# Optimization experiments

Hardware: AMD Instinct MI355X
Metric: run time of the kernel (lower is better)

## Reference

```python
import jax, jax.numpy as jnp
import numpy as np

LEVEL = 4
INV_SQRT2 = np.float32(0.7071067811865476)  # db1 (Haar) filter coefficient


def haar_dwt(x):
    # pywt db1 single-level DWT for even-length signals (symmetric mode reduces
    # to this for the 2-tap Haar filter): cA[k]=(x[2k]+x[2k+1])/sqrt2,
    # cD[k]=(x[2k]-x[2k+1])/sqrt2
    xe = x[..., 0::2]
    xo = x[..., 1::2]
    cA = (xe + xo) * INV_SQRT2
    cD = (xe - xo) * INV_SQRT2
    return cA, cD


def haar_idwt(cA, cD):
    # inverse: x[2k]=(cA+cD)/sqrt2, x[2k+1]=(cA-cD)/sqrt2, interleaved
    even = (cA + cD) * INV_SQRT2
    odd = (cA - cD) * INV_SQRT2
    out = jnp.stack([even, odd], axis=-1)  # [..., n/2, 2]
    return out.reshape(*cA.shape[:-1], cA.shape[-1] * 2)


def setup_inputs() -> dict:
    key = jax.random.key(0)
    x = jax.random.normal(key, (32, 512, 4096), dtype=jnp.float32)
    return {"x": x}


def reference(x):
    # pywt.wavedec(x, 'db1', level=4): recursive DWT on approximation coeffs
    cA = x
    details = []
    for _ in range(LEVEL):
        cA, cD = haar_dwt(cA)
        details.append(cD)
    # pywt.waverec: reconstruct from [cA_L, cD_L, ..., cD_1]
    for cD in reversed(details):
        cA = haar_idwt(cA, cD)
    return cA
```

## Files before the change

### kernel.cpp

```cpp
#include <hip/hip_runtime.h>


#define WBLK 16

__global__ __launch_bounds__(256) void wavelet_rt_kernel(
    const float4* __restrict__ in, float4* __restrict__ out, int nthreads) {
  int t = blockIdx.x * blockDim.x + threadIdx.x;
  if (t >= nthreads) return;

  const float S = 0.7071067811865476f;

  float v[16];
  #pragma unroll
  for (int k = 0; k < 4; ++k) {
    float4 r = in[t * 4 + k];
    v[4 * k + 0] = r.x; v[4 * k + 1] = r.y;
    v[4 * k + 2] = r.z; v[4 * k + 3] = r.w;
  }

  float a1[8], d1[8];
  #pragma unroll
  for (int i = 0; i < 8; ++i) {
    float e = v[2 * i], o = v[2 * i + 1];
    a1[i] = (e + o) * S;
    d1[i] = (e - o) * S;
  }
  float a2[4], d2[4];
  #pragma unroll
  for (int i = 0; i < 4; ++i) {
    float e = a1[2 * i], o = a1[2 * i + 1];
    a2[i] = (e + o) * S;
    d2[i] = (e - o) * S;
  }
  float a3[2], d3[2];
  #pragma unroll
  for (int i = 0; i < 2; ++i) {
    float e = a2[2 * i], o = a2[2 * i + 1];
    a3[i] = (e + o) * S;
    d3[i] = (e - o) * S;
  }
  float a4 = (a3[0] + a3[1]) * S;
  float d4 = (a3[0] - a3[1]) * S;

  float b3[2];
  b3[0] = (a4 + d4) * S;
  b3[1] = (a4 - d4) * S;
  float b2[4];
  #pragma unroll
  for (int i = 0; i < 2; ++i) {
    b2[2 * i + 0] = (b3[i] + d3[i]) * S;
    b2[2 * i + 1] = (b3[i] - d3[i]) * S;
  }
  float b1[8];
  #pragma unroll
  for (int i = 0; i < 4; ++i) {
    b1[2 * i + 0] = (b2[i] + d2[i]) * S;
    b1[2 * i + 1] = (b2[i] - d2[i]) * S;
  }
  float w[16];
  #pragma unroll
  for (int i = 0; i < 8; ++i) {
    w[2 * i + 0] = (b1[i] + d1[i]) * S;
    w[2 * i + 1] = (b1[i] - d1[i]) * S;
  }

  #pragma unroll
  for (int k = 0; k < 4; ++k) {
    float4 o4;
    o4.x = w[4 * k + 0]; o4.y = w[4 * k + 1];
    o4.z = w[4 * k + 2]; o4.w = w[4 * k + 3];
    out[t * 4 + k] = o4;
  }
}

extern "C" void kernel_launch(void* const* d_in, const int* in_sizes, int n_in,
                              void* d_out, int out_size, void* d_ws, size_t ws_size,
                              hipStream_t stream) {
  const float* x = (const float*)d_in[0];
  float* out = (float*)d_out;
  int nthreads = out_size / WBLK;
  int block = 256;
  int grid = (nthreads + block - 1) / block;
  wavelet_rt_kernel<<<grid, block, 0, stream>>>(
      (const float4*)x, (float4*)out, nthreads);
}
```

Baseline: 437.9 us.

## Split each 16-element Haar block across four lanes using wavefront shuffles

Each thread now handles one float4 instead of four, and the coarser DWT levels are computed across neighbouring lanes via __shfl_xor exchanges. This makes every global load and store fully coalesced across the wavefront instead of 64-byte strided per lane. It quadruples the thread count and adds shuffle and select instructions.

```diff
diff --git a/kernel.cpp b/kernel.cpp
--- a/kernel.cpp
+++ b/kernel.cpp
@@ -1,7 +1,5 @@
 #include <hip/hip_runtime.h>
 
-
-#define WBLK 16
 
 __global__ __launch_bounds__(256) void wavelet_rt_kernel(
     const float4* __restrict__ in, float4* __restrict__ out, int nthreads) {
@@ -9,68 +7,34 @@
   if (t >= nthreads) return;
 
   const float S = 0.7071067811865476f;
+  const int lane = threadIdx.x & 63;
 
-  float v[16];
-  #pragma unroll
-  for (int k = 0; k < 4; ++k) {
-    float4 r = in[t * 4 + k];
-    v[4 * k + 0] = r.x; v[4 * k + 1] = r.y;
-    v[4 * k + 2] = r.z; v[4 * k + 3] = r.w;
-  }
+  float4 r = in[t];
+  float v0 = r.x, v1 = r.y, v2 = r.z, v3 = r.w;
 
-  float a1[8], d1[8];
-  #pragma unroll
-  for (int i = 0; i < 8; ++i) {
-    float e = v[2 * i], o = v[2 * i + 1];
-    a1[i] = (e + o) * S;
-    d1[i] = (e - o) * S;
-  }
-  float a2[4], d2[4];
-  #pragma unroll
-  for (int i = 0; i < 4; ++i) {
-    float e = a1[2 * i], o = a1[2 * i + 1];
-    a2[i] = (e + o) * S;
-    d2[i] = (e - o) * S;
-  }
-  float a3[2], d3[2];
-  #pragma unroll
-  for (int i = 0; i < 2; ++i) {
-    float e = a2[2 * i], o = a2[2 * i + 1];
-    a3[i] = (e + o) * S;
-    d3[i] = (e - o) * S;
-  }
-  float a4 = (a3[0] + a3[1]) * S;
-  float d4 = (a3[0] - a3[1]) * S;
+  float a1_0 = (v0 + v1) * S, d1_0 = (v0 - v1) * S;
+  float a1_1 = (v2 + v3) * S, d1_1 = (v2 - v3) * S;
+  float a2 = (a1_0 + a1_1) * S, d2 = (a1_0 - a1_1) * S;
+  float p1 = __shfl_xor(a2, 1);
+  float e3 = (lane & 1) ? p1 : a2;
+  float o3 = (lane & 1) ? a2 : p1;
+  float a3 = (e3 + o3) * S, d3 = (e3 - o3) * S;
+  float p2 = __shfl_xor(a3, 2);
+  float e4 = (lane & 2) ? p2 : a3;
+  float o4 = (lane & 2) ? a3 : p2;
+  float a4 = (e4 + o4) * S, d4 = (e4 - o4) * S;
 
-  float b3[2];
-  b3[0] = (a4 + d4) * S;
-  b3[1] = (a4 - d4) * S;
-  float b2[4];
-  #pragma unroll
-  for (int i = 0; i < 2; ++i) {
-    b2[2 * i + 0] = (b3[i] + d3[i]) * S;
-    b2[2 * i + 1] = (b3[i] - d3[i]) * S;
-  }
-  float b1[8];
-  #pragma unroll
-  for (int i = 0; i < 4; ++i) {
-    b1[2 * i + 0] = (b2[i] + d2[i]) * S;
-    b1[2 * i + 1] = (b2[i] - d2[i]) * S;
-  }
-  float w[16];
-  #pragma unroll
-  for (int i = 0; i < 8; ++i) {
-    w[2 * i + 0] = (b1[i] + d1[i]) * S;
-    w[2 * i + 1] = (b1[i] - d1[i]) * S;
-  }
+  float b3 = (lane & 2) ? (a4 - d4) * S : (a4 + d4) * S;
+  float b2 = (lane & 1) ? (b3 - d3) * S : (b3 + d3) * S;
+  float b1_0 = (b2 + d2) * S;
+  float b1_1 = (b2 - d2) * S;
+  float4 o4v;
+  o4v.x = (b1_0 + d1_0) * S;
+  o4v.y = (b1_0 - d1_0) * S;
+  o4v.z = (b1_1 + d1_1) * S;
+  o4v.w = (b1_1 - d1_1) * S;
 
-  #pragma unroll
-  for (int k = 0; k < 4; ++k) {
-    float4 o4;
-    o4.x = w[4 * k + 0]; o4.y = w[4 * k + 1];
-    o4.z = w[4 * k + 2]; o4.w = w[4 * k + 3];
-    out[t * 4 + k] = o4;
-  }
+  out[t] = o4v;
 }
 
 extern "C" void kernel_launch(void* const* d_in, const int* in_sizes, int n_in,
@@ -78,7 +42,7 @@
                               hipStream_t stream) {
   const float* x = (const float*)d_in[0];
   float* out = (float*)d_out;
-  int nthreads = out_size / WBLK;
+  int nthreads = out_size / 4;
   int block = 256;
   int grid = (nthreads + block - 1) / block;
   wavelet_rt_kernel<<<grid, block, 0, stream>>>(
```

After: 409.2 us. 1.07x faster.
